# Kernel tuning notes

Measured on AMD Instinct MI355X. Metric: run time of the kernel, lower is better.

Reference implementation:

```python
import math
import jax, jax.numpy as jnp
import numpy as np

HIDDEN = 1024   # config.hidden_size
INTER = 4096    # config.intermediate_size
EXPERTS = 8     # config.moe_experts == config.global_experts
B, T = 4, 2048
EPS = 1e-12     # config.epsilon
CAP_FACTOR = 1.0
MIN_CAP = 4


def layer_norm(x, g, b, eps=EPS):
    m = jnp.mean(x, axis=-1, keepdims=True)
    v = jnp.var(x, axis=-1, keepdims=True)
    return (x - m) * jax.lax.rsqrt(v + eps) * g + b


def top1_gate(x, wg, capacity):
    # DeepSpeed top1gating: softmax gate, argmax expert, capacity-based token drop.
    logits = x @ wg                                    # [S, E]
    gates = jax.nn.softmax(logits, axis=-1)
    E = wg.shape[-1]
    idx = jnp.argmax(gates, axis=-1)                   # [S]
    mask1 = jax.nn.one_hot(idx, E, dtype=gates.dtype)  # [S, E]
    locations = jnp.cumsum(mask1, axis=0) - mask1      # exclusive cumsum = slot within expert
    mask1 = mask1 * (locations < capacity).astype(gates.dtype)  # drop overflow tokens
    gates1_s = jnp.sum(gates * mask1, axis=-1)         # [S] prob of chosen expert
    loc_s = jnp.sum(locations * mask1, axis=-1).astype(jnp.int32)
    loc_oh = jax.nn.one_hot(loc_s, capacity, dtype=gates.dtype)          # [S, C]
    combine = gates1_s[:, None, None] * mask1[:, :, None] * loc_oh[:, None, :]  # [S, E, C]
    dispatch = jax.lax.stop_gradient((combine > 0).astype(x.dtype))      # bool mask in torch
    return combine, dispatch


def setup_inputs() -> dict:
    key = jax.random.key(0)
    ks = jax.random.split(key, 8)
    s = 0.02
    return {
        "x": jax.random.normal(ks[0], (B, T, HIDDEN), jnp.float32),
        "attn_nw": jnp.ones((HIDDEN,), jnp.float32),
        "attn_nb": jnp.zeros((HIDDEN,), jnp.float32),
        "wg": jax.random.normal(ks[1], (HIDDEN, EXPERTS), jnp.float32) * s,
        "inter_w": jax.random.normal(ks[2], (EXPERTS, HIDDEN, INTER), jnp.float32) * s,
        "inter_b": jnp.zeros((EXPERTS, INTER), jnp.float32),
        "output_w": jax.random.normal(ks[3], (EXPERTS, INTER, HIDDEN), jnp.float32) * s,
        "output_b": jnp.zeros((EXPERTS, HIDDEN), jnp.float32),
        "res_inter_w": jax.random.normal(ks[4], (HIDDEN, INTER), jnp.float32) * s,
        "res_inter_b": jnp.zeros((INTER,), jnp.float32),
        "res_output_w": jax.random.normal(ks[5], (INTER, HIDDEN), jnp.float32) * s,
        "res_output_b": jnp.zeros((HIDDEN,), jnp.float32),
        "res_coef": jax.random.normal(ks[6], (HIDDEN, 2), jnp.float32) * s,
    }


def reference(x, attn_nw, attn_nb, wg, inter_w, inter_b, output_w, output_b,
              res_inter_w, res_inter_b, res_output_w, res_output_b, res_coef):
    Bx, Tx, M = x.shape
    S = Bx * Tx
    E = wg.shape[-1]
    capacity = max(MIN_CAP, math.ceil(S / E * CAP_FACTOR))  # static

    residual = x.reshape(S, M)                  # attention output + bias (attention = identity here)
    attn_out = layer_norm(residual, attn_nw, attn_nb)  # ds_layernorm

    # gate + dispatch: einsum_sec_sm_ecm
    combine, dispatch = top1_gate(attn_out, wg, capacity)
    dispatched = jnp.einsum('sec,sm->ecm', dispatch, attn_out)  # [E, C, M]

    # expert MLPs: fused gemm-gelu then output projection + bias
    h = jax.nn.gelu(jnp.einsum('ecm,emi->eci', dispatched, inter_w) + inter_b[:, None, :], approximate=True)
    expert_out = jnp.einsum('eci,eim->ecm', h, output_w) + output_b[:, None, :]

    # gated combine: matmul(combine.reshape(S, E*C), expert_out.reshape(E*C, M))
    moe_out = jnp.einsum('sec,ecm->sm', combine, expert_out)

    # residual-MLP branch (mlp_type == 'residual')
    rh = jax.nn.gelu(attn_out @ res_inter_w + res_inter_b, approximate=True)
    res_mlp_out = rh @ res_output_w + res_output_b
    coef = jax.nn.softmax(attn_out @ res_coef, axis=-1)          # [S, 2]
    out = res_mlp_out * coef[:, :1] + moe_out * coef[:, 1:]      # moe_res_matmul

    out = out + residual                                         # bias_residual
    return out.reshape(Bx, Tx, M)
```

## Files before the change

kernel.cpp:

```cpp
#include <hip/hip_runtime.h>
#include <hip/hip_bf16.h>
#include <type_traits>

#define S_TOK 8192
#define HID 1024
#define INTERX 4096
#define NEXP 8
#define CAPX 1024
#define MTOT 16384

using f32x4 = __attribute__((ext_vector_type(4))) float;
using bf16x8 = __attribute__((ext_vector_type(8))) short;

__device__ __forceinline__ short f2bf(float f) {
    union { float f; unsigned u; } v; v.f = f;
    unsigned r = (v.u + 0x7FFFu + ((v.u >> 16) & 1u)) >> 16;
    return (short)r;
}
__device__ __forceinline__ float bflo(int p) {
    union { unsigned u; float f; } v; v.u = (unsigned)p << 16; return v.f;
}
__device__ __forceinline__ float bfhi(int p) {
    union { unsigned u; float f; } v; v.u = (unsigned)p & 0xffff0000u; return v.f;
}

__device__ __forceinline__ float gelu_f(float x) {
    float u = 0.7978845608028654f * (x + 0.044715f * x * x * x);
    float e = __expf(2.0f * u);
    return 0.5f * x * (2.0f - 2.0f / (e + 1.0f));
}

__device__ __forceinline__ void gl_lds16(const short* g, short* l) {
    __builtin_amdgcn_global_load_lds(
        (const __attribute__((address_space(1))) void*)g,
        (__attribute__((address_space(3))) void*)l, 16, 0, 0);
}

__global__ __launch_bounds__(256) void convtrans_kernel(
    const float* __restrict__ src_e, const float* __restrict__ src_r,
    short* __restrict__ dst, int K, int N, long sSrc, long sDst)
{
    __shared__ __align__(16) short tile[64][72];
    long z = blockIdx.z;
    const float* s = (z < 8) ? (src_e + z * sSrc) : src_r;
    short* d = dst + z * sDst;
    int n0 = blockIdx.x * 64, k0 = blockIdx.y * 64;
    int t = threadIdx.x;
    int br = t >> 4, bc = t & 15;
    const float* sp = s + (long)(k0 + br * 4) * N + n0 + bc * 4;
    float4 r0 = *(const float4*)(sp);
    float4 r1 = *(const float4*)(sp + N);
    float4 r2 = *(const float4*)(sp + 2 * (long)N);
    float4 r3 = *(const float4*)(sp + 3 * (long)N);
    short4 c0 = { f2bf(r0.x), f2bf(r1.x), f2bf(r2.x), f2bf(r3.x) };
    short4 c1 = { f2bf(r0.y), f2bf(r1.y), f2bf(r2.y), f2bf(r3.y) };
    short4 c2 = { f2bf(r0.z), f2bf(r1.z), f2bf(r2.z), f2bf(r3.z) };
    short4 c3 = { f2bf(r0.w), f2bf(r1.w), f2bf(r2.w), f2bf(r3.w) };
    *(short4*)&tile[bc * 4 + 0][br * 4] = c0;
    *(short4*)&tile[bc * 4 + 1][br * 4] = c1;
    *(short4*)&tile[bc * 4 + 2][br * 4] = c2;
    *(short4*)&tile[bc * 4 + 3][br * 4] = c3;
    __syncthreads();
    int n = t >> 2, kc = (t & 3) * 16;
    int4 o0 = *(const int4*)&tile[n][kc];
    int4 o1 = *(const int4*)&tile[n][kc + 8];
    short* dp = d + (long)(n0 + n) * K + k0 + kc;
    *(int4*)(dp) = o0;
    *(int4*)(dp + 8) = o1;
}

__global__ __launch_bounds__(256) void ln_gate_kernel(
    const float* __restrict__ x, const float* __restrict__ nw, const float* __restrict__ nb,
    const float* __restrict__ wg, const float* __restrict__ rcf,
    short* __restrict__ attn_bf, int* __restrict__ eidx, float* __restrict__ gate,
    float* __restrict__ coef0, float* __restrict__ coef1)
{
    int s = blockIdx.x, tid = threadIdx.x;
    int lane = tid & 63, wave = tid >> 6;
    __shared__ float wred[4][2];
    __shared__ double gred[4][10];

    float4 xv = *(const float4*)(x + (size_t)s * HID + tid * 4);
    float sum = xv.x + xv.y + xv.z + xv.w;
    float sq  = xv.x*xv.x + xv.y*xv.y + xv.z*xv.z + xv.w*xv.w;
#pragma unroll
    for (int o = 32; o > 0; o >>= 1) {
        sum += __shfl_down(sum, o, 64);
        sq  += __shfl_down(sq, o, 64);
    }
    if (lane == 0) { wred[wave][0] = sum; wred[wave][1] = sq; }
    __syncthreads();
    float ts = wred[0][0] + wred[1][0] + wred[2][0] + wred[3][0];
    float tq = wred[0][1] + wred[1][1] + wred[2][1] + wred[3][1];
    float m  = ts * (1.0f / HID);
    float var = tq * (1.0f / HID) - m * m;
    float rs = rsqrtf(var + 1e-12f);

    float4 g4 = *(const float4*)(nw + tid * 4);
    float4 b4 = *(const float4*)(nb + tid * 4);
    float y[4];
    y[0] = (xv.x - m) * rs * g4.x + b4.x;
    y[1] = (xv.y - m) * rs * g4.y + b4.y;
    y[2] = (xv.z - m) * rs * g4.z + b4.z;
    y[3] = (xv.w - m) * rs * g4.w + b4.w;

    short4 yb = { f2bf(y[0]), f2bf(y[1]), f2bf(y[2]), f2bf(y[3]) };
    *(short4*)(attn_bf + (size_t)s * HID + tid * 4) = yb;

    double a[10];
#pragma unroll
    for (int q = 0; q < 10; q++) a[q] = 0.0;
#pragma unroll
    for (int j = 0; j < 4; j++) {
        int k = tid * 4 + j;
        float4 w0 = *(const float4*)(wg + k * 8);
        float4 w1 = *(const float4*)(wg + k * 8 + 4);
        double yj = (double)y[j];
        a[0] += yj * w0.x; a[1] += yj * w0.y; a[2] += yj * w0.z; a[3] += yj * w0.w;
        a[4] += yj * w1.x; a[5] += yj * w1.y; a[6] += yj * w1.z; a[7] += yj * w1.w;
        float2 rc = *(const float2*)(rcf + k * 2);
        a[8] += yj * rc.x; a[9] += yj * rc.y;
    }
#pragma unroll
    for (int o = 32; o > 0; o >>= 1)
#pragma unroll
        for (int q = 0; q < 10; q++) a[q] += __shfl_down(a[q], o, 64);
    if (lane == 0)
#pragma unroll
        for (int q = 0; q < 10; q++) gred[wave][q] = a[q];
    __syncthreads();
    if (tid == 0) {
        float l[8];
#pragma unroll
        for (int e = 0; e < 8; e++)
            l[e] = (float)(gred[0][e] + gred[1][e] + gred[2][e] + gred[3][e]);
        int bi = 0; float bv = l[0];
#pragma unroll
        for (int e = 1; e < 8; e++) if (l[e] > bv) { bv = l[e]; bi = e; }
        float den = 0.0f;
#pragma unroll
        for (int e = 0; e < 8; e++) den += expf(l[e] - bv);
        gate[s] = 1.0f / den;
        eidx[s] = bi;
        float r0 = (float)(gred[0][8] + gred[1][8] + gred[2][8] + gred[3][8]);
        float r1 = (float)(gred[0][9] + gred[1][9] + gred[2][9] + gred[3][9]);
        float mx = fmaxf(r0, r1);
        float e0 = expf(r0 - mx), e1 = expf(r1 - mx);
        float inv = 1.0f / (e0 + e1);
        coef0[s] = e0 * inv; coef1[s] = e1 * inv;
    }
}

__global__ __launch_bounds__(256) void assign_kernel(
    const int* __restrict__ eidx, int* __restrict__ slot, int* __restrict__ map2,
    short* __restrict__ zbuf)
{
    int tid = threadIdx.x;
    for (int i = tid; i < NEXP * CAPX; i += 256) map2[i] = -1;
    for (int i = tid; i < S_TOK; i += 256) map2[NEXP * CAPX + i] = i;
    for (int i = tid; i < 512; i += 256) ((int*)zbuf)[i] = 0;

    __shared__ int cnt[2][256][NEXP];
    int c[NEXP];
#pragma unroll
    for (int e = 0; e < NEXP; e++) c[e] = 0;
    int base = tid * 32;
    for (int t = 0; t < 32; t++) { int e = eidx[base + t]; c[e]++; }
#pragma unroll
    for (int e = 0; e < NEXP; e++) cnt[0][tid][e] = c[e];
    __syncthreads();

    int src = 0;
    for (int step = 1; step < 256; step <<= 1) {
        int dst = src ^ 1;
#pragma unroll
        for (int e = 0; e < NEXP; e++) {
            int v = cnt[src][tid][e];
            if (tid >= step) v += cnt[src][tid - step][e];
            cnt[dst][tid][e] = v;
        }
        __syncthreads();
        src = dst;
    }
    int off[NEXP];
#pragma unroll
    for (int e = 0; e < NEXP; e++) off[e] = (tid > 0) ? cnt[src][tid - 1][e] : 0;
    for (int t = 0; t < 32; t++) {
        int s = base + t;
        int e = eidx[s];
        int loc = off[e]++;
        if (loc < CAPX) { slot[s] = loc; map2[e * CAPX + loc] = s; }
        else            { slot[s] = -1; }
    }
}

template<int EPI, int GATHER, typename OUT_T>
__global__ __launch_bounds__(256) void gemm_kernel(
    const short* __restrict__ A, const short* __restrict__ W,
    const float* __restrict__ bias_e, const float* __restrict__ bias_r,
    OUT_T* __restrict__ out, const int* __restrict__ map2,
    const short* __restrict__ zbuf, int N, int K, long sW, long sB)
{
    __shared__ __align__(16) short a_lds[128 * 64];
    __shared__ __align__(16) short b_lds[128 * 64];

    int L = blockIdx.x + gridDim.x * blockIdx.y;
    int by = (L & 7) * 16 + ((L >> 3) & 15);
    int bx = L >> 7;

    long e = by >> 3; if (e > 8) e = 8;
    const short* Wb = W + e * sW;
    const float* biasb = (by < 64) ? (bias_e + e * sB) : bias_r;

    int tid = threadIdx.x;
    int lane = tid & 63, wave = tid >> 6;
    int wm = wave & 1, wn = wave >> 1;
    int lm = lane & 15, lq = lane >> 4;
    int lr = lane >> 3, ch = lane & 7;
    int chs = (ch ^ lr) * 8;

    const short* pA[4];
    const short* pB[4];
#pragma unroll
    for (int it = 0; it < 4; it++) {
        int g = wave * 4 + it;
        int row = g * 8 + lr;
        if (GATHER) {
            int s = map2[by * 128 + row];
            pA[it] = (s >= 0) ? (A + (long)s * K) : zbuf;
        } else {
            pA[it] = A + ((long)by * 128 + row) * K;
        }
        pB[it] = Wb + ((long)bx * 128 + row) * K;
    }

    f32x4 acc[4][4];
#pragma unroll
    for (int i = 0; i < 4; i++)
#pragma unroll
        for (int j = 0; j < 4; j++) acc[i][j] = { 0.f, 0.f, 0.f, 0.f };

    int poffA = ((lq ^ (lm & 7)) * 8);

    for (int kb = 0; kb < K; kb += 64) {
#pragma unroll
        for (int it = 0; it < 4; it++) {
            int g = wave * 4 + it;
            gl_lds16(pA[it] + kb + chs, a_lds + g * 512);
            gl_lds16(pB[it] + kb + chs, b_lds + g * 512);
        }
        __syncthreads();
#pragma unroll
        for (int ks = 0; ks < 64; ks += 32) {
            int po = poffA ^ ks;
            bf16x8 af[4], bfr[4];
#pragma unroll
            for (int i = 0; i < 4; i++)
                af[i] = *(const bf16x8*)(a_lds + (wm * 64 + i * 16 + lm) * 64 + po);
#pragma unroll
            for (int j = 0; j < 4; j++)
                bfr[j] = *(const bf16x8*)(b_lds + (wn * 64 + j * 16 + lm) * 64 + po);
#pragma unroll
            for (int i = 0; i < 4; i++)
#pragma unroll
                for (int j = 0; j < 4; j++)
                    acc[i][j] = __builtin_amdgcn_mfma_f32_16x16x32_bf16(af[i], bfr[j], acc[i][j], 0, 0, 0);
        }
        __syncthreads();
    }

    float bb[4];
#pragma unroll
    for (int j = 0; j < 4; j++)
        bb[j] = biasb[bx * 128 + wn * 64 + j * 16 + lm];
#pragma unroll
    for (int i = 0; i < 4; i++) {
#pragma unroll
        for (int r = 0; r < 4; r++) {
            int row = by * 128 + wm * 64 + i * 16 + lq * 4 + r;
#pragma unroll
            for (int j = 0; j < 4; j++) {
                int col = bx * 128 + wn * 64 + j * 16 + lm;
                float v = acc[i][j][r] + bb[j];
                if (EPI == 1) v = gelu_f(v);
                if constexpr (std::is_same_v<OUT_T, short>)
                    out[(long)row * N + col] = f2bf(v);
                else
                    out[(long)row * N + col] = v;
            }
        }
    }
}

__global__ __launch_bounds__(256) void final_kernel(
    const float* __restrict__ x, const short* __restrict__ eout2,
    const int* __restrict__ eidx, const int* __restrict__ slot,
    const float* __restrict__ gate, const float* __restrict__ coef0,
    const float* __restrict__ coef1, float* __restrict__ out)
{
    int s = blockIdx.x, tid = threadIdx.x;
    float c0 = coef0[s], g = gate[s] * coef1[s];
    int sl = slot[s], e = eidx[s];
    float4 xv = *(const float4*)(x + (size_t)s * HID + tid * 4);
    int2 rm = *(const int2*)(eout2 + ((size_t)(NEXP * CAPX + s)) * HID + tid * 4);
    int2 mo = { 0, 0 };
    if (sl >= 0) mo = *(const int2*)(eout2 + ((size_t)(e * CAPX + sl)) * HID + tid * 4);
    float4 o;
    o.x = bflo(rm.x) * c0 + g * bflo(mo.x) + xv.x;
    o.y = bfhi(rm.x) * c0 + g * bfhi(mo.x) + xv.y;
    o.z = bflo(rm.y) * c0 + g * bflo(mo.y) + xv.z;
    o.w = bfhi(rm.y) * c0 + g * bfhi(mo.y) + xv.w;
    *(float4*)(out + (size_t)s * HID + tid * 4) = o;
}

extern "C" void kernel_launch(void* const* d_in, const int* in_sizes, int n_in,
                              void* d_out, int out_size, void* d_ws, size_t ws_size,
                              hipStream_t stream) {
    const float* x           = (const float*)d_in[0];
    const float* attn_nw     = (const float*)d_in[1];
    const float* attn_nb     = (const float*)d_in[2];
    const float* wg          = (const float*)d_in[3];
    const float* inter_w     = (const float*)d_in[4];
    const float* inter_b     = (const float*)d_in[5];
    const float* output_w    = (const float*)d_in[6];
    const float* output_b    = (const float*)d_in[7];
    const float* res_inter_w = (const float*)d_in[8];
    const float* res_inter_b = (const float*)d_in[9];
    const float* res_output_w= (const float*)d_in[10];
    const float* res_output_b= (const float*)d_in[11];
    const float* res_coef    = (const float*)d_in[12];
    float* out = (float*)d_out;

    char* ws = (char*)d_ws;
    size_t off = 0;
    auto alloc = [&](size_t bytes) { void* p = ws + off; off += (bytes + 255) & ~(size_t)255; return p; };
    char* region1 = (char*)alloc((size_t)MTOT * HID * 2);
    short* wreg   = (short*)alloc((size_t)9 * HID * INTERX * 2);
    short* hbuf2  = (short*)alloc((size_t)MTOT * INTERX * 2);
    int*   eidx   = (int*)alloc(S_TOK * 4);
    int*   slot   = (int*)alloc(S_TOK * 4);
    float* gate   = (float*)alloc(S_TOK * 4);
    float* c0     = (float*)alloc(S_TOK * 4);
    float* c1     = (float*)alloc(S_TOK * 4);
    int*   map2   = (int*)alloc(MTOT * 4);
    short* zbuf   = (short*)alloc(1024 * 2);

    short* attn_bf = (short*)region1;
    short* eout2   = (short*)region1;
    short* w1t = wreg;
    short* w2t = wreg;

    convtrans_kernel<<<dim3(INTERX/64, HID/64, 9), 256, 0, stream>>>(
        inter_w, res_inter_w, w1t, HID, INTERX, (long)HID*INTERX, (long)HID*INTERX);

    ln_gate_kernel<<<S_TOK, 256, 0, stream>>>(x, attn_nw, attn_nb, wg, res_coef,
                                              attn_bf, eidx, gate, c0, c1);
    assign_kernel<<<1, 256, 0, stream>>>(eidx, slot, map2, zbuf);

    gemm_kernel<1, 1, short><<<dim3(INTERX/128, 128), 256, 0, stream>>>(
        attn_bf, w1t, inter_b, res_inter_b, hbuf2, map2, zbuf,
        INTERX, HID, (long)HID*INTERX, INTERX);

    convtrans_kernel<<<dim3(HID/64, INTERX/64, 9), 256, 0, stream>>>(
        output_w, res_output_w, w2t, INTERX, HID, (long)INTERX*HID, (long)INTERX*HID);

    gemm_kernel<0, 0, short><<<dim3(HID/128, 128), 256, 0, stream>>>(
        hbuf2, w2t, output_b, res_output_b, eout2, nullptr, nullptr,
        HID, INTERX, (long)INTERX*HID, HID);

    final_kernel<<<S_TOK, 256, 0, stream>>>(x, eout2, eidx, slot, gate, c0, c1, out);

    (void)in_sizes; (void)n_in; (void)out_size; (void)ws_size;
}
```

Before: 872.9 us.

## Widen GEMM tiles to 128x256, permute W2 layout for packed GELU stores

Both expert GEMMs now use a 128x256 output tile per block: B is staged into a doubled LDS buffer and each wave holds a 4x8 accumulator grid. This raises arithmetic intensity and cuts how often A is reloaded. The first GEMM's GELU epilogue writes four bf16 values per 8-byte store in a permuted column order, and the second weight conversion permutes K to match, so the stores are wider and more coalesced. GELU is rewritten as x*sigmoid with a hardware reciprocal, and the map2/zbuf initialisation moves out of the single-block assign kernel into the parallel LN/gate kernel. The risks are higher register pressure under launch_bounds(256,2), with possible spills or lower occupancy, and fewer blocks for the second GEMM.

```diff
diff --git a/kernel.cpp b/kernel.cpp
--- a/kernel.cpp
+++ b/kernel.cpp
@@ -25,9 +25,9 @@
 }
 
 __device__ __forceinline__ float gelu_f(float x) {
-    float u = 0.7978845608028654f * (x + 0.044715f * x * x * x);
-    float e = __expf(2.0f * u);
-    return 0.5f * x * (2.0f - 2.0f / (e + 1.0f));
+    float x2 = x * x;
+    float t = __expf(x * fmaf(x2, -0.07135677f, -1.5957691f));
+    return x * __builtin_amdgcn_rcpf(1.0f + t);
 }
 
 __device__ __forceinline__ void gl_lds16(const short* g, short* l) {
@@ -36,6 +36,7 @@
         (__attribute__((address_space(3))) void*)l, 16, 0, 0);
 }
 
+template<int PERM>
 __global__ __launch_bounds__(256) void convtrans_kernel(
     const float* __restrict__ src_e, const float* __restrict__ src_r,
     short* __restrict__ dst, int K, int N, long sSrc, long sDst)
@@ -52,14 +53,27 @@
     float4 r1 = *(const float4*)(sp + N);
     float4 r2 = *(const float4*)(sp + 2 * (long)N);
     float4 r3 = *(const float4*)(sp + 3 * (long)N);
-    short4 c0 = { f2bf(r0.x), f2bf(r1.x), f2bf(r2.x), f2bf(r3.x) };
-    short4 c1 = { f2bf(r0.y), f2bf(r1.y), f2bf(r2.y), f2bf(r3.y) };
-    short4 c2 = { f2bf(r0.z), f2bf(r1.z), f2bf(r2.z), f2bf(r3.z) };
-    short4 c3 = { f2bf(r0.w), f2bf(r1.w), f2bf(r2.w), f2bf(r3.w) };
-    *(short4*)&tile[bc * 4 + 0][br * 4] = c0;
-    *(short4*)&tile[bc * 4 + 1][br * 4] = c1;
-    *(short4*)&tile[bc * 4 + 2][br * 4] = c2;
-    *(short4*)&tile[bc * 4 + 3][br * 4] = c3;
+    if (PERM) {
+        float rr[4][4] = { {r0.x,r0.y,r0.z,r0.w}, {r1.x,r1.y,r1.z,r1.w},
+                           {r2.x,r2.y,r2.z,r2.w}, {r3.x,r3.y,r3.z,r3.w} };
+#pragma unroll
+        for (int j = 0; j < 4; j++) {
+            int kl = br * 4 + j;
+            int kp = (kl & 15) * 4 + (kl >> 4);
+#pragma unroll
+            for (int q = 0; q < 4; q++)
+                tile[bc * 4 + q][kp] = f2bf(rr[j][q]);
+        }
+    } else {
+        short4 c0 = { f2bf(r0.x), f2bf(r1.x), f2bf(r2.x), f2bf(r3.x) };
+        short4 c1 = { f2bf(r0.y), f2bf(r1.y), f2bf(r2.y), f2bf(r3.y) };
+        short4 c2 = { f2bf(r0.z), f2bf(r1.z), f2bf(r2.z), f2bf(r3.z) };
+        short4 c3 = { f2bf(r0.w), f2bf(r1.w), f2bf(r2.w), f2bf(r3.w) };
+        *(short4*)&tile[bc * 4 + 0][br * 4] = c0;
+        *(short4*)&tile[bc * 4 + 1][br * 4] = c1;
+        *(short4*)&tile[bc * 4 + 2][br * 4] = c2;
+        *(short4*)&tile[bc * 4 + 3][br * 4] = c3;
+    }
     __syncthreads();
     int n = t >> 2, kc = (t & 3) * 16;
     int4 o0 = *(const int4*)&tile[n][kc];
@@ -73,12 +87,19 @@
     const float* __restrict__ x, const float* __restrict__ nw, const float* __restrict__ nb,
     const float* __restrict__ wg, const float* __restrict__ rcf,
     short* __restrict__ attn_bf, int* __restrict__ eidx, float* __restrict__ gate,
-    float* __restrict__ coef0, float* __restrict__ coef1)
+    float* __restrict__ coef0, float* __restrict__ coef1,
+    int* __restrict__ map2, int* __restrict__ zbufi)
 {
     int s = blockIdx.x, tid = threadIdx.x;
     int lane = tid & 63, wave = tid >> 6;
     __shared__ float wred[4][2];
     __shared__ double gred[4][10];
+
+    if (tid == 0) {
+        map2[s] = -1;
+        map2[NEXP * CAPX + s] = s;
+    }
+    if (s == 0) ((int2*)zbufi)[tid] = int2{0, 0};
 
     float4 xv = *(const float4*)(x + (size_t)s * HID + tid * 4);
     float sum = xv.x + xv.y + xv.z + xv.w;
@@ -152,14 +173,9 @@
 }
 
 __global__ __launch_bounds__(256) void assign_kernel(
-    const int* __restrict__ eidx, int* __restrict__ slot, int* __restrict__ map2,
-    short* __restrict__ zbuf)
+    const int* __restrict__ eidx, int* __restrict__ slot, int* __restrict__ map2)
 {
     int tid = threadIdx.x;
-    for (int i = tid; i < NEXP * CAPX; i += 256) map2[i] = -1;
-    for (int i = tid; i < S_TOK; i += 256) map2[NEXP * CAPX + i] = i;
-    for (int i = tid; i < 512; i += 256) ((int*)zbuf)[i] = 0;
-
     __shared__ int cnt[2][256][NEXP];
     int c[NEXP];
 #pragma unroll
@@ -194,15 +210,15 @@
     }
 }
 
-template<int EPI, int GATHER, typename OUT_T>
-__global__ __launch_bounds__(256) void gemm_kernel(
+template<int EPI, int GATHER>
+__global__ __launch_bounds__(256, 2) void gemm_kernel(
     const short* __restrict__ A, const short* __restrict__ W,
     const float* __restrict__ bias_e, const float* __restrict__ bias_r,
-    OUT_T* __restrict__ out, const int* __restrict__ map2,
+    short* __restrict__ out, const int* __restrict__ map2,
     const short* __restrict__ zbuf, int N, int K, long sW, long sB)
 {
     __shared__ __align__(16) short a_lds[128 * 64];
-    __shared__ __align__(16) short b_lds[128 * 64];
+    __shared__ __align__(16) short b_lds[256 * 64];
 
     int L = blockIdx.x + gridDim.x * blockIdx.y;
     int by = (L & 7) * 16 + ((L >> 3) & 15);
@@ -220,73 +236,85 @@
     int chs = (ch ^ lr) * 8;
 
     const short* pA[4];
-    const short* pB[4];
+    const short* pB[8];
 #pragma unroll
     for (int it = 0; it < 4; it++) {
-        int g = wave * 4 + it;
-        int row = g * 8 + lr;
+        int row = (wave * 4 + it) * 8 + lr;
         if (GATHER) {
             int s = map2[by * 128 + row];
             pA[it] = (s >= 0) ? (A + (long)s * K) : zbuf;
         } else {
             pA[it] = A + ((long)by * 128 + row) * K;
         }
-        pB[it] = Wb + ((long)bx * 128 + row) * K;
-    }
-
-    f32x4 acc[4][4];
+    }
+#pragma unroll
+    for (int it = 0; it < 8; it++) {
+        int row = (wave * 8 + it) * 8 + lr;
+        pB[it] = Wb + ((long)bx * 256 + row) * K;
+    }
+
+    f32x4 acc[4][8];
 #pragma unroll
     for (int i = 0; i < 4; i++)
 #pragma unroll
-        for (int j = 0; j < 4; j++) acc[i][j] = { 0.f, 0.f, 0.f, 0.f };
-
-    int poffA = ((lq ^ (lm & 7)) * 8);
+        for (int j = 0; j < 8; j++) acc[i][j] = { 0.f, 0.f, 0.f, 0.f };
 
     for (int kb = 0; kb < K; kb += 64) {
 #pragma unroll
-        for (int it = 0; it < 4; it++) {
-            int g = wave * 4 + it;
-            gl_lds16(pA[it] + kb + chs, a_lds + g * 512);
-            gl_lds16(pB[it] + kb + chs, b_lds + g * 512);
-        }
+        for (int it = 0; it < 4; it++)
+            gl_lds16(pA[it] + kb + chs, a_lds + (wave * 4 + it) * 512);
+#pragma unroll
+        for (int it = 0; it < 8; it++)
+            gl_lds16(pB[it] + kb + chs, b_lds + (wave * 8 + it) * 512);
         __syncthreads();
 #pragma unroll
         for (int ks = 0; ks < 64; ks += 32) {
-            int po = poffA ^ ks;
-            bf16x8 af[4], bfr[4];
+            int po = ((lq ^ (lm & 7)) * 8) ^ ks;
+            bf16x8 af[4], bfr[8];
 #pragma unroll
             for (int i = 0; i < 4; i++)
                 af[i] = *(const bf16x8*)(a_lds + (wm * 64 + i * 16 + lm) * 64 + po);
 #pragma unroll
-            for (int j = 0; j < 4; j++)
-                bfr[j] = *(const bf16x8*)(b_lds + (wn * 64 + j * 16 + lm) * 64 + po);
+            for (int j = 0; j < 8; j++)
+                bfr[j] = *(const bf16x8*)(b_lds + (wn * 128 + j * 16 + lm) * 64 + po);
 #pragma unroll
             for (int i = 0; i < 4; i++)
 #pragma unroll
-                for (int j = 0; j < 4; j++)
+                for (int j = 0; j < 8; j++)
                     acc[i][j] = __builtin_amdgcn_mfma_f32_16x16x32_bf16(af[i], bfr[j], acc[i][j], 0, 0, 0);
         }
         __syncthreads();
     }
 
-    float bb[4];
-#pragma unroll
-    for (int j = 0; j < 4; j++)
-        bb[j] = biasb[bx * 128 + wn * 64 + j * 16 + lm];
+    float bb[8];
+#pragma unroll
+    for (int j = 0; j < 8; j++)
+        bb[j] = biasb[bx * 256 + wn * 128 + j * 16 + lm];
+
 #pragma unroll
     for (int i = 0; i < 4; i++) {
 #pragma unroll
         for (int r = 0; r < 4; r++) {
-            int row = by * 128 + wm * 64 + i * 16 + lq * 4 + r;
-#pragma unroll
-            for (int j = 0; j < 4; j++) {
-                int col = bx * 128 + wn * 64 + j * 16 + lm;
-                float v = acc[i][j][r] + bb[j];
-                if (EPI == 1) v = gelu_f(v);
-                if constexpr (std::is_same_v<OUT_T, short>)
-                    out[(long)row * N + col] = f2bf(v);
-                else
-                    out[(long)row * N + col] = v;
+            long row = (long)by * 128 + wm * 64 + i * 16 + lq * 4 + r;
+            if (EPI == 1) {
+                short* rp = out + row * N + bx * 256 + wn * 128;
+#pragma unroll
+                for (int h = 0; h < 2; h++) {
+                    int b0 = f2bf(gelu_f(acc[i][h*4+0][r] + bb[h*4+0]));
+                    int b1 = f2bf(gelu_f(acc[i][h*4+1][r] + bb[h*4+1]));
+                    int b2 = f2bf(gelu_f(acc[i][h*4+2][r] + bb[h*4+2]));
+                    int b3 = f2bf(gelu_f(acc[i][h*4+3][r] + bb[h*4+3]));
+                    int2 pk;
+                    pk.x = (b0 & 0xFFFF) | (b1 << 16);
+                    pk.y = (b2 & 0xFFFF) | (b3 << 16);
+                    *(int2*)(rp + h * 64 + lm * 4) = pk;
+                }
+            } else {
+#pragma unroll
+                for (int j = 0; j < 8; j++) {
+                    int col = bx * 256 + wn * 128 + j * 16 + lm;
+                    out[row * N + col] = f2bf(acc[i][j][r] + bb[j]);
+                }
             }
         }
     }
@@ -350,22 +378,23 @@
     short* w1t = wreg;
     short* w2t = wreg;
 
-    convtrans_kernel<<<dim3(INTERX/64, HID/64, 9), 256, 0, stream>>>(
+    convtrans_kernel<0><<<dim3(INTERX/64, HID/64, 9), 256, 0, stream>>>(
         inter_w, res_inter_w, w1t, HID, INTERX, (long)HID*INTERX, (long)HID*INTERX);
 
     ln_gate_kernel<<<S_TOK, 256, 0, stream>>>(x, attn_nw, attn_nb, wg, res_coef,
-                                              attn_bf, eidx, gate, c0, c1);
-    assign_kernel<<<1, 256, 0, stream>>>(eidx, slot, map2, zbuf);
-
-    gemm_kernel<1, 1, short><<<dim3(INTERX/128, 128), 256, 0, stream>>>(
+                                              attn_bf, eidx, gate, c0, c1,
+                                              map2, (int*)zbuf);
+    assign_kernel<<<1, 256, 0, stream>>>(eidx, slot, map2);
+
+    gemm_kernel<1, 1><<<dim3(INTERX/256, 128), 256, 0, stream>>>(
         attn_bf, w1t, inter_b, res_inter_b, hbuf2, map2, zbuf,
         INTERX, HID, (long)HID*INTERX, INTERX);
 
-    convtrans_kernel<<<dim3(HID/64, INTERX/64, 9), 256, 0, stream>>>(
+    convtrans_kernel<1><<<dim3(HID/64, INTERX/64, 9), 256, 0, stream>>>(
         output_w, res_output_w, w2t, INTERX, HID, (long)INTERX*HID, (long)INTERX*HID);
 
-    gemm_kernel<0, 0, short><<<dim3(HID/128, 128), 256, 0, stream>>>(
-        hbuf2, w2t, output_b, res_output_b, eout2, nullptr, nullptr,
+    gemm_kernel<0, 0><<<dim3(HID/256, 128), 256, 0, stream>>>(
+        hbuf2, w2t, output_b, res_output_b, eout2, nullptr, zbuf,
         HID, INTERX, (long)INTERX*HID, HID);
 
     final_kernel<<<S_TOK, 256, 0, stream>>>(x, eout2, eidx, slot, gate, c0, c1, out);
```

New measurement: 732.8 us. -16.1%, faster.
